# Optimization experiments

Hardware: AMD Instinct MI355X
Metric: run time of the kernel (lower is better)

The kernel has to match this reference:

```python
import jax, jax.numpy as jnp
import numpy as np

H = 1024      # hidden_size
P = 32        # num_props -> output dim 2P=64
E = 8         # num_experts
C = 4         # num_centroids
K = 2         # top_k
B = 16384     # batch
TEMP = 0.1

def _glorot(key, shape):
    fan_in, fan_out = shape[-2], shape[-1]
    lim = jnp.sqrt(6.0 / (fan_in + fan_out))
    return jax.random.uniform(key, shape, jnp.float32, -lim, lim)

def setup_inputs() -> dict:
    key = jax.random.key(0)
    ks = jax.random.split(key, 16)
    return {
        'multimodal_feat': jax.random.normal(ks[0], (B, H), jnp.float32),
        'query_feat': jax.random.normal(ks[1], (B, H), jnp.float32),
        'ln_gamma': jnp.ones((H,), jnp.float32),
        'ln_beta': jnp.zeros((H,), jnp.float32),
        'pilot_emb': _glorot(ks[2], (E, C, H)),
        'qproj_W': _glorot(ks[3], (2 * H, H)),
        'qproj_b': jnp.zeros((H,), jnp.float32),
        'eW1': _glorot(ks[4], (E, H, H)),
        'eb1': jnp.zeros((E, H), jnp.float32),
        'eW2': _glorot(ks[5], (E, H, 2 * P)),
        'eb2': jnp.zeros((E, 2 * P), jnp.float32),
        'sW1': _glorot(ks[6], (H, H)),
        'sb1': jnp.zeros((H,), jnp.float32),
        'sW2': _glorot(ks[7], (H, 2 * P)),
        'sb2': jnp.zeros((2 * P,), jnp.float32),
        'gate_W': _glorot(ks[8], (4 * P, 2 * P)),
        'gate_b': jnp.zeros((2 * P,), jnp.float32),
    }

def _layer_norm(x, g, b, eps=1e-5):
    mu = jnp.mean(x, axis=-1, keepdims=True)
    var = jnp.var(x, axis=-1, keepdims=True)
    return (x - mu) * jax.lax.rsqrt(var + eps) * g + b

def _l2norm(x, axis=-1, eps=1e-12):
    n = jnp.linalg.norm(x, axis=axis, keepdims=True)
    return x / jnp.maximum(n, eps)

def reference(multimodal_feat, query_feat, ln_gamma, ln_beta, pilot_emb,
              qproj_W, qproj_b, eW1, eb1, eW2, eb2,
              sW1, sb1, sW2, sb2, gate_W, gate_b):
    bsz = multimodal_feat.shape[0]
    x = _layer_norm(multimodal_feat, ln_gamma, ln_beta)  # [B,H]

    # --- router ---
    fused = jnp.concatenate([x, query_feat], axis=-1)        # [B,2H]
    q = _l2norm(fused @ qproj_W + qproj_b)                   # [B,H]
    pilots = _l2norm(pilot_emb)                              # [E,C,H]
    sims = jnp.einsum('bh,ech->bec', q, pilots)              # [B,E,C]
    expert_scores = sims.mean(axis=-1)                       # [B,E]
    expert_probs = jax.nn.softmax(expert_scores / TEMP, axis=-1)
    topk_w, topk_idx = jax.lax.top_k(expert_probs, K)        # [B,K]
    topk_w = topk_w / (topk_w.sum(axis=-1, keepdims=True) + 1e-6)

    # combine weights per expert: [B,E]
    onehot = jax.nn.one_hot(topk_idx, E, dtype=x.dtype)      # [B,K,E]
    cw = jnp.einsum('bk,bke->be', topk_w, onehot)            # [B,E]

    # --- routed experts (dense all-expert compute, weighted combine) ---
    h = jax.nn.relu(jnp.einsum('bh,ehd->ebd', x, eW1) + eb1[:, None, :])  # [E,B,H]
    eout = jnp.einsum('ebd,edp->ebp', h, eW2) + eb2[:, None, :]           # [E,B,2P]
    routed = jnp.einsum('be,ebp->bp', cw, eout)                           # [B,2P]

    # --- shared expert + gate ---
    sh = jax.nn.relu(x @ sW1 + sb1)
    shared = sh @ sW2 + sb2                                   # [B,2P]
    combined = jnp.concatenate([routed, shared], axis=-1)     # [B,4P]
    out = combined @ gate_W + gate_b                          # [B,2P]

    gauss_params = jax.nn.sigmoid(out).reshape(bsz * P, 2)
    return gauss_params
```

## Files before the change

kernel.cpp:

```cpp
#include <hip/hip_runtime.h>
#include <hip/hip_bf16.h>
#include <stdint.h>

typedef unsigned short u16;
typedef __attribute__((ext_vector_type(8))) short short8;
typedef __attribute__((ext_vector_type(4))) float f32x4;

#define NB 16384
#define NH 1024
#define NSLOT 49152
#define NCHUNK 4

static __device__ __forceinline__ u16 f2bf(float f){
  union { float f; uint32_t u; } a; a.f = f;
  return (u16)((a.u + 0x7fffu + ((a.u >> 16) & 1u)) >> 16);
}

static __device__ __forceinline__ void gld16(const u16* gsrc, u16* lds){
  __builtin_amdgcn_global_load_lds((const __attribute__((address_space(1))) void*)gsrc,
                                   (__attribute__((address_space(3))) void*)lds, 16, 0, 0);
}

__global__ __launch_bounds__(256) void k_token_prep(
    const float* __restrict__ mm, const float* __restrict__ qf,
    const float* __restrict__ gamma, const float* __restrict__ beta,
    u16* __restrict__ fusedb, float* __restrict__ mu, float* __restrict__ rstd)
{
  int b = blockIdx.x, t = threadIdx.x;
  __shared__ float red[16];
  float4 v = ((const float4*)(mm + (size_t)b*NH))[t];
  float s = v.x+v.y+v.z+v.w;
  for (int o=32;o;o>>=1) s += __shfl_down(s,o);
  int wid = t>>6, lane = t&63;
  if (!lane) red[wid] = s;
  __syncthreads();
  if (t==0) red[8] = (red[0]+red[1]+red[2]+red[3]) * (1.0f/NH);
  __syncthreads();
  float mean = red[8];
  float4 d; d.x=v.x-mean; d.y=v.y-mean; d.z=v.z-mean; d.w=v.w-mean;
  float s2 = d.x*d.x+d.y*d.y+d.z*d.z+d.w*d.w;
  for (int o=32;o;o>>=1) s2 += __shfl_down(s2,o);
  if (!lane) red[4+wid] = s2;
  __syncthreads();
  if (t==0) red[9] = rsqrtf((red[4]+red[5]+red[6]+red[7])*(1.0f/NH) + 1e-5f);
  __syncthreads();
  float rs = red[9];
  if (t==0){ mu[b]=mean; rstd[b]=rs; }
  float4 g = ((const float4*)gamma)[t], be = ((const float4*)beta)[t];
  ushort4 ox;
  ox.x = f2bf(d.x*rs*g.x+be.x); ox.y = f2bf(d.y*rs*g.y+be.y);
  ox.z = f2bf(d.z*rs*g.z+be.z); ox.w = f2bf(d.w*rs*g.w+be.w);
  ((ushort4*)(fusedb + (size_t)b*2048))[t] = ox;
  float4 q = ((const float4*)(qf + (size_t)b*NH))[t];
  ushort4 oq; oq.x=f2bf(q.x); oq.y=f2bf(q.y); oq.z=f2bf(q.z); oq.w=f2bf(q.w);
  ((ushort4*)(fusedb + (size_t)b*2048 + 1024))[t] = oq;
}

__global__ __launch_bounds__(256) void k_pilots(const float* __restrict__ pe, float* __restrict__ pn)
{
  int ec = blockIdx.x, t = threadIdx.x;
  __shared__ double dred[8];
  float4 v = ((const float4*)(pe + (size_t)ec*NH))[t];
  double s2 = (double)v.x*v.x + (double)v.y*v.y + (double)v.z*v.z + (double)v.w*v.w;
  for (int o=32;o;o>>=1) s2 += __shfl_down(s2,o);
  int wid=t>>6, lane=t&63;
  if (!lane) dred[wid]=s2;
  __syncthreads();
  if (t==0) dred[4] = 1.0 / fmax(sqrt(dred[0]+dred[1]+dred[2]+dred[3]), 1e-12);
  __syncthreads();
  double inv = dred[4];
  float4 o; o.x=(float)(v.x*inv); o.y=(float)(v.y*inv); o.z=(float)(v.z*inv); o.w=(float)(v.w*inv);
  ((float4*)(pn + (size_t)ec*NH))[t] = o;
}

__global__ __launch_bounds__(256) void k_M(const float* __restrict__ W, const float* __restrict__ pn,
                                           double* __restrict__ M)
{
  int j = blockIdx.x;
  __shared__ float wrow[NH];
  __shared__ double part[256];
  for (int i=threadIdx.x;i<NH;i+=256) wrow[i] = W[(size_t)j*NH + i];
  __syncthreads();
  int ec = threadIdx.x>>3, seg = threadIdx.x&7;
  const float* p = pn + (size_t)ec*NH + seg*128;
  const float* wr = wrow + seg*128;
  double a = 0;
  #pragma unroll 8
  for (int i=0;i<128;i++) a += (double)wr[i]*(double)p[i];
  part[threadIdx.x] = a;
  __syncthreads();
  if (seg==0){
    double s=0;
    for (int i=0;i<8;i++) s += part[(ec<<3)+i];
    M[(size_t)j*32 + ec] = s;
  }
}

__global__ __launch_bounds__(256) void k_smalls(
    const float* eb1, const float* sb1, const float* eb2, const float* sb2,
    const float* gW, const float* gb, const float* qb, const float* pn,
    float* b1_all, float* cvec, double* cr)
{
  int idx = blockIdx.x*256 + threadIdx.x;
  if (idx < 9216){
    int e = idx>>10, k = idx&1023;
    b1_all[idx] = (e<8) ? eb1[idx] : sb1[k];
  } else if (idx < 9216+576){
    int i = idx-9216; int e = i>>6, n = i&63;
    float a = (e<8) ? 0.0f : gb[n];
    for (int j=0;j<64;j++){
      float bj = (e<8) ? eb2[e*64+j] : sb2[j];
      a += bj * gW[(((e<8)?j:64+j))*64 + n];
    }
    cvec[i] = a;
  } else if (idx < 9216+576+32){
    int ec = idx-9216-576;
    double a=0;
    for (int h=0;h<NH;h++) a += (double)qb[h]*(double)pn[(size_t)ec*NH+h];
    cr[ec] = a;
  }
}

__global__ __launch_bounds__(256) void k_transpose_bf16(const float* __restrict__ src, u16* __restrict__ dst,
                                                        int K, int N)
{
  __shared__ float tile[32][33];
  int k0 = blockIdx.x*32, n0 = blockIdx.y*32;
  int tx = threadIdx.x & 31, ty = threadIdx.x >> 5;
  for (int i=0;i<4;i++) tile[ty+i*8][tx] = src[(size_t)(k0+ty+i*8)*N + n0 + tx];
  __syncthreads();
  for (int i=0;i<4;i++) dst[(size_t)(n0+ty+i*8)*K + k0 + tx] = f2bf(tile[tx][ty+i*8]);
}

__global__ __launch_bounds__(256) void k_w1t(const float* __restrict__ eW1, const float* __restrict__ sW1,
                                             u16* __restrict__ w1t)
{
  __shared__ float tile[32][33];
  int e = blockIdx.z;
  const float* src = (e<8) ? eW1 + ((size_t)e<<20) : sW1;
  u16* dst = w1t + ((size_t)e<<20);
  int k0 = blockIdx.x*32, n0 = blockIdx.y*32;
  int tx = threadIdx.x & 31, ty = threadIdx.x >> 5;
  for (int i=0;i<4;i++) tile[ty+i*8][tx] = src[(size_t)(k0+ty+i*8)*NH + n0 + tx];
  __syncthreads();
  for (int i=0;i<4;i++) dst[(size_t)(n0+ty+i*8)*NH + k0 + tx] = f2bf(tile[tx][ty+i*8]);
}

__global__ __launch_bounds__(256) void k_fold_w2(const float* __restrict__ eW2, const float* __restrict__ sW2,
                                                 const float* __restrict__ gW, u16* __restrict__ w2t)
{
  __shared__ float gsh[64*64];
  int e = blockIdx.y;
  const float* src = (e<8) ? eW2 + (size_t)e*NH*64 : sW2;
  int rowbase = (e<8) ? 0 : 64;
  for (int i=threadIdx.x;i<64*64;i+=256) gsh[i] = gW[(size_t)(rowbase + (i>>6))*64 + (i&63)];
  __syncthreads();
  int flat = blockIdx.x*256 + threadIdx.x;
  int n = flat >> 10, k = flat & 1023;
  float acc = 0;
  #pragma unroll 8
  for (int j=0;j<64;j++) acc += src[(size_t)k*64 + j] * gsh[j*64 + n];
  w2t[(size_t)e*64*NH + flat] = f2bf(acc);
}

__global__ __launch_bounds__(256) void k_router(
    const float* __restrict__ mm, const float* __restrict__ qf,
    const float* __restrict__ gamma, const float* __restrict__ beta,
    const float* __restrict__ mu, const float* __restrict__ rstd,
    const double* __restrict__ M, double* __restrict__ u_part)
{
  __shared__ float At[16][130];
  __shared__ double Ms[16][32];
  int rb = blockIdx.x * 128;
  int kc = blockIdx.y * 512;
  bool isx = (kc < 1024);
  const float* src = isx ? mm : qf;
  int ksrc = isx ? kc : kc-1024;
  int t = threadIdx.x;
  int kk4 = (t&3)*4, rr = t>>2;
  int rg4 = t & 31, ec0 = (t>>5)*4;
  double acc[4][4] = {};

  for (int kb=0; kb<512; kb+=16){
    __syncthreads();
    float4 g4, b4;
    if (isx){ g4 = *(const float4*)(gamma + kc+kb+kk4); b4 = *(const float4*)(beta + kc+kb+kk4); }
    #pragma unroll
    for (int i=0;i<2;i++){
      int r = rr + i*64;
      float4 v = *(const float4*)(src + (size_t)(rb+r)*NH + ksrc + kb + kk4);
      if (isx){
        float m = mu[rb+r], rs = rstd[rb+r];
        v.x=(v.x-m)*rs*g4.x+b4.x; v.y=(v.y-m)*rs*g4.y+b4.y;
        v.z=(v.z-m)*rs*g4.z+b4.z; v.w=(v.w-m)*rs*g4.w+b4.w;
      }
      At[kk4+0][r]=v.x; At[kk4+1][r]=v.y; At[kk4+2][r]=v.z; At[kk4+3][r]=v.w;
    }
    const double* msrc = M + (size_t)(kc+kb)*32;
    ((double*)Ms)[t]     = msrc[t];
    ((double*)Ms)[256+t] = msrc[256+t];
    __syncthreads();
    #pragma unroll
    for (int kk=0; kk<16; kk++){
      float a4[4]; double m4[4];
      #pragma unroll
      for (int i=0;i<4;i++) a4[i] = At[kk][rg4 + 32*i];
      #pragma unroll
      for (int j=0;j<4;j++) m4[j] = Ms[kk][ec0+j];
      #pragma unroll
      for (int i=0;i<4;i++)
        #pragma unroll
        for (int j=0;j<4;j++) acc[i][j] = fma((double)a4[i], m4[j], acc[i][j]);
    }
  }
  double* dst = u_part + ((size_t)blockIdx.y*NB + rb)*32;
  #pragma unroll
  for (int i=0;i<4;i++){
    size_t row = (size_t)(rg4 + 32*i);
    #pragma unroll
    for (int j=0;j<4;j++) dst[row*32 + ec0 + j] = acc[i][j];
  }
}

__global__ __launch_bounds__(256,2) void k_qnorm(
    const u16* __restrict__ fusedb, const u16* __restrict__ wqt,
    const float* __restrict__ qb, float* __restrict__ norm2)
{
  __shared__ __align__(16) u16 As[128*32];
  __shared__ __align__(16) u16 Bs[256*32];
  int nb = blockIdx.x*256, mb = blockIdx.y*128;
  int t = threadIdx.x;
  int r0 = t>>2, c16 = (t&3)*8;
  const u16* ag0 = fusedb + (size_t)(mb+r0)*2048 + c16;
  const u16* ag1 = fusedb + (size_t)(mb+r0+64)*2048 + c16;
  const u16* bg0 = wqt + (size_t)(nb+r0)*2048 + c16;
  int wid=t>>6, lane=t&63, quad=lane>>4, lr=lane&15;
  int wm=(wid&1)*64, wn=(wid>>1)*128;
  f32x4 acc[4][8] = {};
  for (int kb=0;kb<2048;kb+=32){
    __syncthreads();
    gld16(ag0+kb, As + t*8); gld16(ag1+kb, As + 2048 + t*8);
    gld16(bg0+kb,          Bs + t*8);
    gld16(bg0+kb +  64*2048, Bs + 2048 + t*8);
    gld16(bg0+kb + 128*2048, Bs + 4096 + t*8);
    gld16(bg0+kb + 192*2048, Bs + 6144 + t*8);
    __syncthreads();
    short8 af[4], bf[8];
    #pragma unroll
    for (int i=0;i<4;i++) af[i] = *(const short8*)(As + (wm+i*16+lr)*32 + quad*8);
    #pragma unroll
    for (int j=0;j<8;j++) bf[j] = *(const short8*)(Bs + (wn+j*16+lr)*32 + quad*8);
    #pragma unroll
    for (int i=0;i<4;i++)
      #pragma unroll
      for (int j=0;j<8;j++)
        acc[i][j] = __builtin_amdgcn_mfma_f32_16x16x32_bf16(af[i], bf[j], acc[i][j], 0,0,0);
  }
  float qbv[8];
  #pragma unroll
  for (int j=0;j<8;j++) qbv[j] = qb[nb + wn + j*16 + lr];
  float rsum[4][4];
  #pragma unroll
  for (int i=0;i<4;i++)
    #pragma unroll
    for (int r=0;r<4;r++){
      float s=0;
      #pragma unroll
      for (int j=0;j<8;j++){
        float v = acc[i][j][r] + qbv[j];
        s += v*v;
      }
      rsum[i][r]=s;
    }
  #pragma unroll
  for (int m=1;m<16;m<<=1)
    #pragma unroll
    for (int i=0;i<4;i++)
      #pragma unroll
      for (int r=0;r<4;r++) rsum[i][r] += __shfl_xor(rsum[i][r], m);
  if (lr==0){
    #pragma unroll
    for (int i=0;i<4;i++)
      #pragma unroll
      for (int r=0;r<4;r++)
        unsafeAtomicAdd(&norm2[mb + wm + i*16 + quad*4 + r], rsum[i][r]);
  }
}

__global__ __launch_bounds__(256) void k_scores(
    const double* __restrict__ u_part, const double* __restrict__ cr, const float* __restrict__ norm2,
    int2* __restrict__ idx2, float2* __restrict__ w12, int* __restrict__ counts)
{
  __shared__ int lcnt[8];
  int t = threadIdx.x;
  if (t<8) lcnt[t]=0;
  __syncthreads();
  int b = blockIdx.x*256 + t;
  double s[8];
  #pragma unroll
  for (int e=0;e<8;e++) s[e] = cr[e*4]+cr[e*4+1]+cr[e*4+2]+cr[e*4+3];
  for (int c=0;c<NCHUNK;c++){
    const double* up = u_part + ((size_t)c*NB + b)*32;
    #pragma unroll
    for (int e=0;e<8;e++) s[e] += up[e*4]+up[e*4+1]+up[e*4+2]+up[e*4+3];
  }
  double inv = 0.25 / fmax(sqrt((double)norm2[b]), 1e-12);
  #pragma unroll
  for (int e=0;e<8;e++) s[e] *= inv;
  int e1 = 0;
  for (int e=1;e<8;e++) if (s[e] > s[e1]) e1 = e;
  int e2 = (e1==0) ? 1 : 0;
  for (int e=0;e<8;e++) if (e!=e1 && s[e] > s[e2]) e2 = e;
  double mx = s[e1], S = 0, p[8];
  #pragma unroll
  for (int e=0;e<8;e++){ p[e] = exp((s[e]-mx)*10.0); S += p[e]; }
  double P1 = p[e1]/S, P2 = p[e2]/S;
  double den = P1 + P2 + 1e-6;
  idx2[b] = make_int2(e1,e2);
  w12[b]  = make_float2((float)(P1/den), (float)(P2/den));
  atomicAdd(&lcnt[e1],1); atomicAdd(&lcnt[e2],1);
  __syncthreads();
  if (t<8) atomicAdd(&counts[t], lcnt[t]);
}

__global__ void k_prefix(const int* counts, int* offs, int* cursor){
  if (threadIdx.x==0 && blockIdx.x==0){
    int o=0;
    for (int e=0;e<8;e++){ offs[e]=o; cursor[e]=o; o+=counts[e]; }
    offs[8]=o;
  }
}

__global__ __launch_bounds__(256) void k_fill(const int2* __restrict__ idx2, const float2* __restrict__ w12,
                                              int* cursor, int* __restrict__ tok_list, float* __restrict__ wt_list)
{
  __shared__ int lc[8], base[8];
  int t = threadIdx.x;
  if (t<8) lc[t]=0;
  __syncthreads();
  int b = blockIdx.x*256 + t;
  int2 e = idx2[b]; float2 w = w12[b];
  int p1 = atomicAdd(&lc[e.x],1);
  int p2 = atomicAdd(&lc[e.y],1);
  __syncthreads();
  if (t<8) base[t] = atomicAdd(&cursor[t], lc[t]);
  __syncthreads();
  int s1 = base[e.x]+p1, s2 = base[e.y]+p2;
  tok_list[s1]=b; wt_list[s1]=w.x;
  tok_list[s2]=b; wt_list[s2]=w.y;
  tok_list[2*NB + b] = b; wt_list[2*NB + b] = 1.0f;
}

__global__ __launch_bounds__(256,2) void k_expert(
    const u16* __restrict__ fusedb, const u16* __restrict__ w1t, const float* __restrict__ b1_all,
    const u16* __restrict__ w2t,
    const int* __restrict__ tok_list, const float* __restrict__ wt_list,
    const int* __restrict__ offs, const int* __restrict__ counts,
    float* __restrict__ out_acc)
{
  int e = blockIdx.z;
  int cnt = (e<8) ? counts[e] : NB;
  int off = (e<8) ? offs[e]   : 2*NB;
  int mb = blockIdx.y * 128;
  if (mb >= cnt) return;
  int rem = cnt - mb;
  int nb = blockIdx.x * 256;
  __shared__ __align__(16) u16 As[128*32];
  __shared__ __align__(16) u16 Bs[256*32];
  __shared__ __align__(16) u16 B2[64*264];
  __shared__ __align__(16) u16 hl[128*72];
  int t = threadIdx.x;

  {
    const u16* wb2 = w2t + (size_t)e*64*NH + nb;
    #pragma unroll
    for (int s=0;s<8;s++){
      int flat = s*256 + t;
      int row = flat>>5, c8 = (flat&31)*8;
      *(uint4*)(B2 + row*264 + c8) = *(const uint4*)(wb2 + (size_t)row*NH + c8);
    }
  }

  int r0 = t>>2, c16 = (t&3)*8;
  int r0c = r0    < rem ? r0    : rem-1;
  int r1c = r0+64 < rem ? r0+64 : rem-1;
  int tok0 = tok_list[off + mb + r0c];
  int tok1 = tok_list[off + mb + r1c];
  const u16* wbase = w1t + ((size_t)e<<20);
  const u16* ag0 = fusedb + (size_t)tok0*2048 + c16;
  const u16* ag1 = fusedb + (size_t)tok1*2048 + c16;
  const u16* bg0 = wbase + (size_t)(nb+r0)*NH + c16;
  int wid=t>>6, lane=t&63, quad=lane>>4, lr=lane&15;
  int wm=(wid&1)*64, wn=(wid>>1)*128;
  f32x4 acc[4][8] = {};
  for (int kb=0;kb<1024;kb+=32){
    __syncthreads();
    gld16(ag0+kb, As + t*8); gld16(ag1+kb, As + 2048 + t*8);
    gld16(bg0+kb,           Bs + t*8);
    gld16(bg0+kb +  64*NH,  Bs + 2048 + t*8);
    gld16(bg0+kb + 128*NH,  Bs + 4096 + t*8);
    gld16(bg0+kb + 192*NH,  Bs + 6144 + t*8);
    __syncthreads();
    short8 af[4], bf[8];
    #pragma unroll
    for (int i=0;i<4;i++) af[i] = *(const short8*)(As + (wm+i*16+lr)*32 + quad*8);
    #pragma unroll
    for (int j=0;j<8;j++) bf[j] = *(const short8*)(Bs + (wn+j*16+lr)*32 + quad*8);
    #pragma unroll
    for (int i=0;i<4;i++)
      #pragma unroll
      for (int j=0;j<8;j++)
        acc[i][j] = __builtin_amdgcn_mfma_f32_16x16x32_bf16(af[i], bf[j], acc[i][j], 0,0,0);
  }

  float b1v[8];
  #pragma unroll
  for (int j=0;j<8;j++) b1v[j] = b1_all[e*NH + nb + wn + j*16 + lr];

  f32x4 acc2[2][4] = {};
  int myhalf = wn>>7;
  #pragma unroll
  for (int jj=0;jj<4;jj++){
    __syncthreads();
    if ((jj>>1) == myhalf){
      int j0 = (jj&1)*4;
      #pragma unroll
      for (int i=0;i<4;i++)
        #pragma unroll
        for (int j2=0;j2<4;j2++)
          #pragma unroll
          for (int reg=0;reg<4;reg++){
            float v = acc[i][j0+j2][reg] + b1v[j0+j2];
            hl[(wm+i*16+quad*4+reg)*72 + j2*16 + lr] = f2bf(fmaxf(v,0.0f));
          }
    }
    __syncthreads();
    #pragma unroll
    for (int kk=0;kk<2;kk++){
      short8 a2[2], b2f[4];
      #pragma unroll
      for (int i2=0;i2<2;i2++)
        a2[i2] = *(const short8*)(hl + (wid*32+i2*16+lr)*72 + kk*32 + quad*8);
      #pragma unroll
      for (int j2=0;j2<4;j2++)
        b2f[j2] = *(const short8*)(B2 + (j2*16+lr)*264 + jj*64 + kk*32 + quad*8);
      #pragma unroll
      for (int i2=0;i2<2;i2++)
        #pragma unroll
        for (int j2=0;j2<4;j2++)
          acc2[i2][j2] = __builtin_amdgcn_mfma_f32_16x16x32_bf16(a2[i2], b2f[j2], acc2[i2][j2], 0,0,0);
    }
  }

  #pragma unroll
  for (int i2=0;i2<2;i2++)
    #pragma unroll
    for (int reg=0;reg<4;reg++){
      int m = wid*32 + i2*16 + quad*4 + reg;
      if (m < rem){
        int slot = off + mb + m;
        int tok = tok_list[slot];
        float w = wt_list[slot];
        float* dst = out_acc + (size_t)tok*64;
        #pragma unroll
        for (int j2=0;j2<4;j2++)
          unsafeAtomicAdd(dst + j2*16 + lr, w * acc2[i2][j2][reg]);
      }
    }
}

__global__ __launch_bounds__(256) void k_final(
    const float* __restrict__ out_acc, const float* __restrict__ cvec,
    const int2* __restrict__ idx2, const float2* __restrict__ w12, float* __restrict__ out)
{
  int i = blockIdx.x*256 + threadIdx.x;
  int b = i>>6, n = i&63;
  int2 e = idx2[b]; float2 w = w12[b];
  float v = out_acc[i] + w.x*cvec[e.x*64+n] + w.y*cvec[e.y*64+n] + cvec[8*64+n];
  out[i] = 1.0f / (1.0f + expf(-v));
}

extern "C" void kernel_launch(void* const* d_in, const int* in_sizes, int n_in,
                              void* d_out, int out_size, void* d_ws, size_t ws_size,
                              hipStream_t stream)
{
  (void)in_sizes; (void)n_in; (void)out_size; (void)ws_size;
  const float* mm   =(const float*)d_in[0];
  const float* qf   =(const float*)d_in[1];
  const float* gamma=(const float*)d_in[2];
  const float* beta =(const float*)d_in[3];
  const float* pe   =(const float*)d_in[4];
  const float* qW   =(const float*)d_in[5];
  const float* qb   =(const float*)d_in[6];
  const float* eW1  =(const float*)d_in[7];
  const float* eb1  =(const float*)d_in[8];
  const float* eW2  =(const float*)d_in[9];
  const float* eb2  =(const float*)d_in[10];
  const float* sW1  =(const float*)d_in[11];
  const float* sb1  =(const float*)d_in[12];
  const float* sW2  =(const float*)d_in[13];
  const float* sb2  =(const float*)d_in[14];
  const float* gW   =(const float*)d_in[15];
  const float* gb   =(const float*)d_in[16];
  float* out = (float*)d_out;

  char* p = (char*)d_ws;
  auto alloc = [&](size_t bytes)->char*{ char* r = p; p += (bytes + 255) & ~(size_t)255; return r; };
  float*  out_acc = (float*) alloc((size_t)NB*64*4);
  float*  norm2   = (float*) alloc((size_t)NB*4);
  int*    counts  = (int*)   alloc(64);
  int*    cursor  = (int*)   alloc(64);
  int*    offs    = (int*)   alloc(64);
  size_t zero_bytes = (size_t)(p - (char*)d_ws);
  double* u_part  = (double*)alloc((size_t)NCHUNK*NB*32*8);
  u16*    fusedb  = (u16*)   alloc((size_t)NB*2048*2);
  u16*    w1t     = (u16*)   alloc((size_t)9*NH*NH*2);
  u16*    wqt     = (u16*)   alloc((size_t)NH*2048*2);
  u16*    w2t     = (u16*)   alloc((size_t)9*64*NH*2);
  float*  b1_all  = (float*) alloc((size_t)9*NH*4);
  float*  cvec    = (float*) alloc((size_t)9*64*4);
  double* M       = (double*)alloc((size_t)2048*32*8);
  float*  pn      = (float*) alloc((size_t)32*NH*4);
  double* cr      = (double*)alloc(32*8);
  float*  mu      = (float*) alloc((size_t)NB*4);
  float*  rstd    = (float*) alloc((size_t)NB*4);
  int2*   idx2    = (int2*)  alloc((size_t)NB*8);
  float2* w12     = (float2*)alloc((size_t)NB*8);
  int*    tok_list= (int*)   alloc((size_t)NSLOT*4);
  float*  wt_list = (float*) alloc((size_t)NSLOT*4);

  hipMemsetAsync(d_ws, 0, zero_bytes, stream);
  k_token_prep<<<NB, 256, 0, stream>>>(mm, qf, gamma, beta, fusedb, mu, rstd);
  k_pilots<<<32, 256, 0, stream>>>(pe, pn);
  k_M<<<2048, 256, 0, stream>>>(qW, pn, M);
  k_smalls<<<39, 256, 0, stream>>>(eb1, sb1, eb2, sb2, gW, gb, qb, pn, b1_all, cvec, cr);
  k_transpose_bf16<<<dim3(64,32), 256, 0, stream>>>(qW, wqt, 2048, 1024);
  k_w1t<<<dim3(32,32,9), 256, 0, stream>>>(eW1, sW1, w1t);
  k_fold_w2<<<dim3(256,9), 256, 0, stream>>>(eW2, sW2, gW, w2t);
  k_qnorm<<<dim3(4,128), 256, 0, stream>>>(fusedb, wqt, qb, norm2);
  k_router<<<dim3(128,NCHUNK), 256, 0, stream>>>(mm, qf, gamma, beta, mu, rstd, M, u_part);
  k_scores<<<64, 256, 0, stream>>>(u_part, cr, norm2, idx2, w12, counts);
  k_prefix<<<1, 64, 0, stream>>>(counts, offs, cursor);
  k_fill<<<64, 256, 0, stream>>>(idx2, w12, cursor, tok_list, wt_list);
  k_expert<<<dim3(4,128,9), 256, 0, stream>>>(fusedb, w1t, b1_all, w2t, tok_list, wt_list, offs, counts, out_acc);
  k_final<<<4096, 256, 0, stream>>>(out_acc, cvec, idx2, w12, out);
}
```

Baseline: 660.9 us.

## Merge router and qnorm kernels, shrink GEMM N-tiles to 128 with smaller LDS

Folds the fp64 router partial-score kernel and the q-projection norm GEMM into one launch of 1536 blocks. Blocks below 512 run the router work and the rest run the qnorm GEMM, so the two independent workloads share the GPU. Both the qnorm GEMM and the expert GEMM drop their N-tile from 256 to 128 columns, which halves accumulator registers and doubles the grid. The expert kernel aliases its LDS buffers and streams its folded W2 slice per 64-column chunk instead of staging the whole 256-wide slice up front. This targets more resident waves and more blocks in flight, at the cost of reloading the A tile twice as often across N-blocks and issuing more atomic adds into norm2 and out_acc.

```diff
diff --git a/kernel.cpp b/kernel.cpp
--- a/kernel.cpp
+++ b/kernel.cpp
@@ -163,127 +163,124 @@
   w2t[(size_t)e*64*NH + flat] = f2bf(acc);
 }
 
-__global__ __launch_bounds__(256) void k_router(
+__global__ __launch_bounds__(256,2) void k_rq(
     const float* __restrict__ mm, const float* __restrict__ qf,
     const float* __restrict__ gamma, const float* __restrict__ beta,
     const float* __restrict__ mu, const float* __restrict__ rstd,
-    const double* __restrict__ M, double* __restrict__ u_part)
-{
-  __shared__ float At[16][130];
-  __shared__ double Ms[16][32];
-  int rb = blockIdx.x * 128;
-  int kc = blockIdx.y * 512;
-  bool isx = (kc < 1024);
-  const float* src = isx ? mm : qf;
-  int ksrc = isx ? kc : kc-1024;
-  int t = threadIdx.x;
-  int kk4 = (t&3)*4, rr = t>>2;
-  int rg4 = t & 31, ec0 = (t>>5)*4;
-  double acc[4][4] = {};
-
-  for (int kb=0; kb<512; kb+=16){
-    __syncthreads();
-    float4 g4, b4;
-    if (isx){ g4 = *(const float4*)(gamma + kc+kb+kk4); b4 = *(const float4*)(beta + kc+kb+kk4); }
-    #pragma unroll
-    for (int i=0;i<2;i++){
-      int r = rr + i*64;
-      float4 v = *(const float4*)(src + (size_t)(rb+r)*NH + ksrc + kb + kk4);
-      if (isx){
-        float m = mu[rb+r], rs = rstd[rb+r];
-        v.x=(v.x-m)*rs*g4.x+b4.x; v.y=(v.y-m)*rs*g4.y+b4.y;
-        v.z=(v.z-m)*rs*g4.z+b4.z; v.w=(v.w-m)*rs*g4.w+b4.w;
-      }
-      At[kk4+0][r]=v.x; At[kk4+1][r]=v.y; At[kk4+2][r]=v.z; At[kk4+3][r]=v.w;
-    }
-    const double* msrc = M + (size_t)(kc+kb)*32;
-    ((double*)Ms)[t]     = msrc[t];
-    ((double*)Ms)[256+t] = msrc[256+t];
-    __syncthreads();
-    #pragma unroll
-    for (int kk=0; kk<16; kk++){
-      float a4[4]; double m4[4];
-      #pragma unroll
-      for (int i=0;i<4;i++) a4[i] = At[kk][rg4 + 32*i];
-      #pragma unroll
-      for (int j=0;j<4;j++) m4[j] = Ms[kk][ec0+j];
-      #pragma unroll
-      for (int i=0;i<4;i++)
-        #pragma unroll
-        for (int j=0;j<4;j++) acc[i][j] = fma((double)a4[i], m4[j], acc[i][j]);
-    }
-  }
-  double* dst = u_part + ((size_t)blockIdx.y*NB + rb)*32;
-  #pragma unroll
-  for (int i=0;i<4;i++){
-    size_t row = (size_t)(rg4 + 32*i);
-    #pragma unroll
-    for (int j=0;j<4;j++) dst[row*32 + ec0 + j] = acc[i][j];
-  }
-}
-
-__global__ __launch_bounds__(256,2) void k_qnorm(
+    const double* __restrict__ M, double* __restrict__ u_part,
     const u16* __restrict__ fusedb, const u16* __restrict__ wqt,
     const float* __restrict__ qb, float* __restrict__ norm2)
 {
-  __shared__ __align__(16) u16 As[128*32];
-  __shared__ __align__(16) u16 Bs[256*32];
-  int nb = blockIdx.x*256, mb = blockIdx.y*128;
+  __shared__ __align__(16) char smem[16384];
   int t = threadIdx.x;
-  int r0 = t>>2, c16 = (t&3)*8;
-  const u16* ag0 = fusedb + (size_t)(mb+r0)*2048 + c16;
-  const u16* ag1 = fusedb + (size_t)(mb+r0+64)*2048 + c16;
-  const u16* bg0 = wqt + (size_t)(nb+r0)*2048 + c16;
-  int wid=t>>6, lane=t&63, quad=lane>>4, lr=lane&15;
-  int wm=(wid&1)*64, wn=(wid>>1)*128;
-  f32x4 acc[4][8] = {};
-  for (int kb=0;kb<2048;kb+=32){
-    __syncthreads();
-    gld16(ag0+kb, As + t*8); gld16(ag1+kb, As + 2048 + t*8);
-    gld16(bg0+kb,          Bs + t*8);
-    gld16(bg0+kb +  64*2048, Bs + 2048 + t*8);
-    gld16(bg0+kb + 128*2048, Bs + 4096 + t*8);
-    gld16(bg0+kb + 192*2048, Bs + 6144 + t*8);
-    __syncthreads();
-    short8 af[4], bf[8];
-    #pragma unroll
-    for (int i=0;i<4;i++) af[i] = *(const short8*)(As + (wm+i*16+lr)*32 + quad*8);
-    #pragma unroll
-    for (int j=0;j<8;j++) bf[j] = *(const short8*)(Bs + (wn+j*16+lr)*32 + quad*8);
+  if (blockIdx.x < 512){
+    float (*At)[130] = (float(*)[130])smem;
+    double (*Ms)[32] = (double(*)[32])(smem + 8320);
+    int rb = (blockIdx.x & 127) * 128;
+    int kc = (blockIdx.x >> 7) * 512;
+    bool isx = (kc < 1024);
+    const float* src = isx ? mm : qf;
+    int ksrc = isx ? kc : kc-1024;
+    int kk4 = (t&3)*4, rr = t>>2;
+    int rg4 = t & 31, ec0 = (t>>5)*4;
+    double acc[4][4] = {};
+    for (int kb=0; kb<512; kb+=16){
+      __syncthreads();
+      float4 g4, b4;
+      if (isx){ g4 = *(const float4*)(gamma + kc+kb+kk4); b4 = *(const float4*)(beta + kc+kb+kk4); }
+      #pragma unroll
+      for (int i=0;i<2;i++){
+        int r = rr + i*64;
+        float4 v = *(const float4*)(src + (size_t)(rb+r)*NH + ksrc + kb + kk4);
+        if (isx){
+          float m = mu[rb+r], rs = rstd[rb+r];
+          v.x=(v.x-m)*rs*g4.x+b4.x; v.y=(v.y-m)*rs*g4.y+b4.y;
+          v.z=(v.z-m)*rs*g4.z+b4.z; v.w=(v.w-m)*rs*g4.w+b4.w;
+        }
+        At[kk4+0][r]=v.x; At[kk4+1][r]=v.y; At[kk4+2][r]=v.z; At[kk4+3][r]=v.w;
+      }
+      const double* msrc = M + (size_t)(kc+kb)*32;
+      ((double*)Ms)[t]     = msrc[t];
+      ((double*)Ms)[256+t] = msrc[256+t];
+      __syncthreads();
+      #pragma unroll
+      for (int kk=0; kk<16; kk++){
+        float a4[4]; double m4[4];
+        #pragma unroll
+        for (int i=0;i<4;i++) a4[i] = At[kk][rg4 + 32*i];
+        #pragma unroll
+        for (int j=0;j<4;j++) m4[j] = Ms[kk][ec0+j];
+        #pragma unroll
+        for (int i=0;i<4;i++)
+          #pragma unroll
+          for (int j=0;j<4;j++) acc[i][j] = fma((double)a4[i], m4[j], acc[i][j]);
+      }
+    }
+    double* dst = u_part + ((size_t)(blockIdx.x>>7)*NB + rb)*32;
+    #pragma unroll
+    for (int i=0;i<4;i++){
+      size_t row = (size_t)(rg4 + 32*i);
+      #pragma unroll
+      for (int j=0;j<4;j++) dst[row*32 + ec0 + j] = acc[i][j];
+    }
+  } else {
+    u16* As = (u16*)smem;
+    u16* Bs = (u16*)smem + 4096;
+    int bx = blockIdx.x - 512;
+    int nb = (bx & 7)*128, mb = (bx >> 3)*128;
+    int r0 = t>>2, c16 = (t&3)*8;
+    const u16* ag0 = fusedb + (size_t)(mb+r0)*2048 + c16;
+    const u16* ag1 = fusedb + (size_t)(mb+r0+64)*2048 + c16;
+    const u16* bg0 = wqt + (size_t)(nb+r0)*2048 + c16;
+    const u16* bg1 = wqt + (size_t)(nb+r0+64)*2048 + c16;
+    int wid=t>>6, lane=t&63, quad=lane>>4, lr=lane&15;
+    int wm=(wid&1)*64, wn=(wid>>1)*64;
+    f32x4 acc[4][4] = {};
+    for (int kb=0;kb<2048;kb+=32){
+      __syncthreads();
+      gld16(ag0+kb, As + t*8); gld16(ag1+kb, As + 2048 + t*8);
+      gld16(bg0+kb, Bs + t*8); gld16(bg1+kb, Bs + 2048 + t*8);
+      __syncthreads();
+      short8 af[4], bf[4];
+      #pragma unroll
+      for (int i=0;i<4;i++) af[i] = *(const short8*)(As + (wm+i*16+lr)*32 + quad*8);
+      #pragma unroll
+      for (int j=0;j<4;j++) bf[j] = *(const short8*)(Bs + (wn+j*16+lr)*32 + quad*8);
+      #pragma unroll
+      for (int i=0;i<4;i++)
+        #pragma unroll
+        for (int j=0;j<4;j++)
+          acc[i][j] = __builtin_amdgcn_mfma_f32_16x16x32_bf16(af[i], bf[j], acc[i][j], 0,0,0);
+    }
+    float qbv[4];
+    #pragma unroll
+    for (int j=0;j<4;j++) qbv[j] = qb[nb + wn + j*16 + lr];
+    float rsum[4][4];
     #pragma unroll
     for (int i=0;i<4;i++)
       #pragma unroll
-      for (int j=0;j<8;j++)
-        acc[i][j] = __builtin_amdgcn_mfma_f32_16x16x32_bf16(af[i], bf[j], acc[i][j], 0,0,0);
-  }
-  float qbv[8];
-  #pragma unroll
-  for (int j=0;j<8;j++) qbv[j] = qb[nb + wn + j*16 + lr];
-  float rsum[4][4];
-  #pragma unroll
-  for (int i=0;i<4;i++)
-    #pragma unroll
-    for (int r=0;r<4;r++){
-      float s=0;
-      #pragma unroll
-      for (int j=0;j<8;j++){
-        float v = acc[i][j][r] + qbv[j];
-        s += v*v;
+      for (int r=0;r<4;r++){
+        float s=0;
+        #pragma unroll
+        for (int j=0;j<4;j++){
+          float v = acc[i][j][r] + qbv[j];
+          s += v*v;
+        }
+        rsum[i][r]=s;
       }
-      rsum[i][r]=s;
-    }
-  #pragma unroll
-  for (int m=1;m<16;m<<=1)
-    #pragma unroll
-    for (int i=0;i<4;i++)
-      #pragma unroll
-      for (int r=0;r<4;r++) rsum[i][r] += __shfl_xor(rsum[i][r], m);
-  if (lr==0){
-    #pragma unroll
-    for (int i=0;i<4;i++)
-      #pragma unroll
-      for (int r=0;r<4;r++)
-        unsafeAtomicAdd(&norm2[mb + wm + i*16 + quad*4 + r], rsum[i][r]);
+    #pragma unroll
+    for (int m=1;m<16;m<<=1)
+      #pragma unroll
+      for (int i=0;i<4;i++)
+        #pragma unroll
+        for (int r=0;r<4;r++) rsum[i][r] += __shfl_xor(rsum[i][r], m);
+    if (lr==0){
+      #pragma unroll
+      for (int i=0;i<4;i++)
+        #pragma unroll
+        for (int r=0;r<4;r++)
+          unsafeAtomicAdd(&norm2[mb + wm + i*16 + quad*4 + r], rsum[i][r]);
+    }
   }
 }
 
@@ -364,23 +361,15 @@
   int mb = blockIdx.y * 128;
   if (mb >= cnt) return;
   int rem = cnt - mb;
-  int nb = blockIdx.x * 256;
-  __shared__ __align__(16) u16 As[128*32];
-  __shared__ __align__(16) u16 Bs[256*32];
-  __shared__ __align__(16) u16 B2[64*264];
-  __shared__ __align__(16) u16 hl[128*72];
+  int nb = blockIdx.x * 128;
+
+  __shared__ __align__(16) u16 smem[13824];
+  u16* As  = smem;
+  u16* Bs  = smem + 4096;
+  u16* hl  = smem;
+  u16* B2c = smem + 9216;
+
   int t = threadIdx.x;
-
-  {
-    const u16* wb2 = w2t + (size_t)e*64*NH + nb;
-    #pragma unroll
-    for (int s=0;s<8;s++){
-      int flat = s*256 + t;
-      int row = flat>>5, c8 = (flat&31)*8;
-      *(uint4*)(B2 + row*264 + c8) = *(const uint4*)(wb2 + (size_t)row*NH + c8);
-    }
-  }
-
   int r0 = t>>2, c16 = (t&3)*8;
   int r0c = r0    < rem ? r0    : rem-1;
   int r1c = r0+64 < rem ? r0+64 : rem-1;
@@ -390,47 +379,53 @@
   const u16* ag0 = fusedb + (size_t)tok0*2048 + c16;
   const u16* ag1 = fusedb + (size_t)tok1*2048 + c16;
   const u16* bg0 = wbase + (size_t)(nb+r0)*NH + c16;
+  const u16* bg1 = wbase + (size_t)(nb+r0+64)*NH + c16;
   int wid=t>>6, lane=t&63, quad=lane>>4, lr=lane&15;
-  int wm=(wid&1)*64, wn=(wid>>1)*128;
-  f32x4 acc[4][8] = {};
+  int wm=(wid&1)*64, wn=(wid>>1)*64;
+  f32x4 acc[4][4] = {};
   for (int kb=0;kb<1024;kb+=32){
     __syncthreads();
     gld16(ag0+kb, As + t*8); gld16(ag1+kb, As + 2048 + t*8);
-    gld16(bg0+kb,           Bs + t*8);
-    gld16(bg0+kb +  64*NH,  Bs + 2048 + t*8);
-    gld16(bg0+kb + 128*NH,  Bs + 4096 + t*8);
-    gld16(bg0+kb + 192*NH,  Bs + 6144 + t*8);
+    gld16(bg0+kb, Bs + t*8); gld16(bg1+kb, Bs + 2048 + t*8);
     __syncthreads();
-    short8 af[4], bf[8];
+    short8 af[4], bf[4];
     #pragma unroll
     for (int i=0;i<4;i++) af[i] = *(const short8*)(As + (wm+i*16+lr)*32 + quad*8);
     #pragma unroll
-    for (int j=0;j<8;j++) bf[j] = *(const short8*)(Bs + (wn+j*16+lr)*32 + quad*8);
+    for (int j=0;j<4;j++) bf[j] = *(const short8*)(Bs + (wn+j*16+lr)*32 + quad*8);
     #pragma unroll
     for (int i=0;i<4;i++)
       #pragma unroll
-      for (int j=0;j<8;j++)
+      for (int j=0;j<4;j++)
         acc[i][j] = __builtin_amdgcn_mfma_f32_16x16x32_bf16(af[i], bf[j], acc[i][j], 0,0,0);
   }
 
-  float b1v[8];
+  float b1v[4];
   #pragma unroll
-  for (int j=0;j<8;j++) b1v[j] = b1_all[e*NH + nb + wn + j*16 + lr];
+  for (int j=0;j<4;j++) b1v[j] = b1_all[e*NH + nb + wn + j*16 + lr];
 
   f32x4 acc2[2][4] = {};
-  int myhalf = wn>>7;
+  int myjj = wn>>6;
   #pragma unroll
-  for (int jj=0;jj<4;jj++){
+  for (int jj=0;jj<2;jj++){
     __syncthreads();
-    if ((jj>>1) == myhalf){
-      int j0 = (jj&1)*4;
+    {
+      const u16* wb2 = w2t + (size_t)e*64*NH + nb + jj*64;
+      #pragma unroll
+      for (int s=0;s<2;s++){
+        int ff = s*256 + t;
+        int row = ff>>3, c8 = (ff&7)*8;
+        *(uint4*)(B2c + row*72 + c8) = *(const uint4*)(wb2 + (size_t)row*NH + c8);
+      }
+    }
+    if (jj == myjj){
       #pragma unroll
       for (int i=0;i<4;i++)
         #pragma unroll
         for (int j2=0;j2<4;j2++)
           #pragma unroll
           for (int reg=0;reg<4;reg++){
-            float v = acc[i][j0+j2][reg] + b1v[j0+j2];
+            float v = acc[i][j2][reg] + b1v[j2];
             hl[(wm+i*16+quad*4+reg)*72 + j2*16 + lr] = f2bf(fmaxf(v,0.0f));
           }
     }
@@ -443,7 +438,7 @@
         a2[i2] = *(const short8*)(hl + (wid*32+i2*16+lr)*72 + kk*32 + quad*8);
       #pragma unroll
       for (int j2=0;j2<4;j2++)
-        b2f[j2] = *(const short8*)(B2 + (j2*16+lr)*264 + jj*64 + kk*32 + quad*8);
+        b2f[j2] = *(const short8*)(B2c + (j2*16+lr)*72 + kk*32 + quad*8);
       #pragma unroll
       for (int i2=0;i2<2;i2++)
         #pragma unroll
@@ -537,11 +532,10 @@
   k_transpose_bf16<<<dim3(64,32), 256, 0, stream>>>(qW, wqt, 2048, 1024);
   k_w1t<<<dim3(32,32,9), 256, 0, stream>>>(eW1, sW1, w1t);
   k_fold_w2<<<dim3(256,9), 256, 0, stream>>>(eW2, sW2, gW, w2t);
-  k_qnorm<<<dim3(4,128), 256, 0, stream>>>(fusedb, wqt, qb, norm2);
-  k_router<<<dim3(128,NCHUNK), 256, 0, stream>>>(mm, qf, gamma, beta, mu, rstd, M, u_part);
+  k_rq<<<1536, 256, 0, stream>>>(mm, qf, gamma, beta, mu, rstd, M, u_part, fusedb, wqt, qb, norm2);
   k_scores<<<64, 256, 0, stream>>>(u_part, cr, norm2, idx2, w12, counts);
   k_prefix<<<1, 64, 0, stream>>>(counts, offs, cursor);
   k_fill<<<64, 256, 0, stream>>>(idx2, w12, cursor, tok_list, wt_list);
-  k_expert<<<dim3(4,128,9), 256, 0, stream>>>(fusedb, w1t, b1_all, w2t, tok_list, wt_list, offs, counts, out_acc);
+  k_expert<<<dim3(8,128,9), 256, 0, stream>>>(fusedb, w1t, b1_all, w2t, tok_list, wt_list, offs, counts, out_acc);
   k_final<<<4096, 256, 0, stream>>>(out_acc, cvec, idx2, w12, out);
 }
```

New measurement: 695.4 us. 5.2% more time.
